# Kernel tuning notes

Measured on AMD Instinct MI355X. Metric: run time of the kernel, lower is better.

Reference implementation:

```python
import jax, jax.numpy as jnp
import numpy as np

B, L, D_MODEL = 4, 4096, 1024
D_STATE = 16
DT_RANK = D_MODEL // 16  # 64
K = 4  # conv kernel size
EPS = 1e-5


def setup_inputs() -> dict:
    key = jax.random.key(0)
    ks = jax.random.split(key, 8)
    s = 0.02
    f = jax.random.normal(ks[0], (B, L, D_MODEL), dtype=jnp.float32)
    ln_g = jnp.ones((D_MODEL,), jnp.float32)
    ln_b = jnp.zeros((D_MODEL,), jnp.float32)
    Wx = jax.random.normal(ks[1], (D_MODEL, D_MODEL), jnp.float32) * s
    bx = jnp.zeros((D_MODEL,), jnp.float32)
    conv_w = jax.random.normal(ks[2], (D_MODEL, K), jnp.float32) * 0.1
    conv_b = jax.random.normal(ks[3], (D_MODEL,), jnp.float32) * s
    Wxp = jax.random.normal(ks[4], (D_MODEL, DT_RANK + 2 * D_STATE), jnp.float32) * s
    Wdt = jax.random.normal(ks[5], (DT_RANK, D_MODEL), jnp.float32) * s
    # negative bias keeps delta small so the (non-exponentiated) recurrence
    # h = (delta*A)*h + ... stays stable over L=4096 steps (|delta*A| < 1)
    bdt = jnp.full((D_MODEL,), -4.0, jnp.float32)
    A_log = jnp.tile(jnp.log(jnp.arange(1, D_STATE + 1, dtype=jnp.float32)), (D_MODEL, 1))
    Dp = jnp.ones((D_MODEL,), jnp.float32)
    return {"f": f, "ln_g": ln_g, "ln_b": ln_b, "Wx": Wx, "bx": bx,
            "conv_w": conv_w, "conv_b": conv_b, "Wxp": Wxp, "Wdt": Wdt,
            "bdt": bdt, "A_log": A_log, "Dp": Dp}


def reference(f, ln_g, ln_b, Wx, bx, conv_w, conv_b, Wxp, Wdt, bdt, A_log, Dp):
    b, l, d = f.shape
    # LayerNorm
    mu = jnp.mean(f, axis=-1, keepdims=True)
    var = jnp.mean(jnp.square(f - mu), axis=-1, keepdims=True)
    fn = (f - mu) * jax.lax.rsqrt(var + EPS) * ln_g + ln_b
    # input projection
    x = fn @ Wx + bx  # (b, l, d)
    # depthwise causal conv1d (torch pad=3 both sides then truncate to l == left-pad 3)
    xp = jnp.pad(x, ((0, 0), (K - 1, 0), (0, 0)))
    windows = jnp.stack([xp[:, k:k + l, :] for k in range(K)], axis=-1)  # (b, l, d, k)
    x = jnp.einsum('bldk,dk->bld', windows, conv_w) + conv_b
    x = jax.nn.silu(x)
    # selective SSM
    x_dbl = x @ Wxp  # (b, l, dt_rank + 2*n)
    dt = x_dbl[..., :DT_RANK]
    Bm = x_dbl[..., DT_RANK:DT_RANK + D_STATE]
    Cm = x_dbl[..., DT_RANK + D_STATE:]
    delta = jax.nn.softplus(dt @ Wdt + bdt)  # (b, l, d)
    A = -jnp.exp(A_log)  # (d, n)

    def step(h, inp):
        d_t, B_t, C_t, x_t = inp  # (b,d) (b,n) (b,n) (b,d)
        dA = d_t[:, :, None] * A                                  # (b, d, n)
        dB = (d_t * x_t)[:, :, None] * B_t[:, None, :]            # (b, d, n)
        h = dA * h + dB
        y = jnp.einsum('bdn,bn->bd', h, C_t)
        return h, y

    h0 = jnp.zeros((b, d, D_STATE), x.dtype)
    xs = (jnp.swapaxes(delta, 0, 1), jnp.swapaxes(Bm, 0, 1),
          jnp.swapaxes(Cm, 0, 1), jnp.swapaxes(x, 0, 1))
    _, ys = jax.lax.scan(step, h0, xs)  # ys: (l, b, d)
    y = jnp.swapaxes(ys, 0, 1) + x * Dp
    return y
```

## Files before the change

kernel.cpp:

```cpp
#include <hip/hip_runtime.h>
#include <cstdint>
#include <cstddef>

#define D_MODEL 1024
#define SEQ_L   4096
#define BATCH   4
#define NROWS   (BATCH*SEQ_L)
#define DSTATE  16
#define DTRANK  64
#define NDBL    96
#define CLEN    64
#define WARM    8
#define CT      16

typedef __attribute__((ext_vector_type(8))) _Float16 f16x8;
typedef __attribute__((ext_vector_type(4))) _Float16 h4;
typedef __attribute__((ext_vector_type(8))) _Float16 h8;
typedef __attribute__((ext_vector_type(4))) float f32x4;
typedef __attribute__((ext_vector_type(2))) float f32x2;

typedef __attribute__((address_space(1))) const unsigned int* as1_u32p;
typedef __attribute__((address_space(3))) unsigned int* as3_u32p;

__device__ __forceinline__ void gload16(const void* g, void* l) {
  __builtin_amdgcn_global_load_lds((as1_u32p)g, (as3_u32p)l, 16, 0, 0);
}

__device__ __forceinline__ float silu(float v) {
  return v / (1.f + __expf(-v));
}

__device__ __forceinline__ float softplus(float z) {
  return (z > 20.f) ? z : __logf(1.f + __expf(z));
}

__device__ __forceinline__ int swz64(int r, int e) { return e ^ ((r & 7) << 3); }

__global__ __launch_bounds__(256) void ln_kernel(const float* __restrict__ f,
                                                 const float* __restrict__ g,
                                                 const float* __restrict__ bta,
                                                 _Float16* __restrict__ fnb) {
  int row = blockIdx.x;
  int tid = threadIdx.x;
  const float* fr = f + (size_t)row * D_MODEL;
  float4 v = *(const float4*)&fr[tid * 4];
  float s  = v.x + v.y + v.z + v.w;
  float ss = v.x*v.x + v.y*v.y + v.z*v.z + v.w*v.w;
  #pragma unroll
  for (int o = 32; o > 0; o >>= 1) { s += __shfl_down(s, o); ss += __shfl_down(ss, o); }
  __shared__ float rs[8];
  int lane = tid & 63, w = tid >> 6;
  if (lane == 0) { rs[w] = s; rs[4 + w] = ss; }
  __syncthreads();
  if (tid == 0) {
    float S = rs[0] + rs[1] + rs[2] + rs[3];
    float SS = rs[4] + rs[5] + rs[6] + rs[7];
    float mu = S * (1.f / D_MODEL);
    float var = SS * (1.f / D_MODEL) - mu * mu;
    rs[0] = mu; rs[1] = rsqrtf(var + 1e-5f);
  }
  __syncthreads();
  float mu = rs[0], rstd = rs[1];
  float4 gv = *(const float4*)&g[tid * 4];
  float4 bv = *(const float4*)&bta[tid * 4];
  h4 o;
  o.x = (_Float16)((v.x - mu) * rstd * gv.x + bv.x);
  o.y = (_Float16)((v.y - mu) * rstd * gv.y + bv.y);
  o.z = (_Float16)((v.z - mu) * rstd * gv.z + bv.z);
  o.w = (_Float16)((v.w - mu) * rstd * gv.w + bv.w);
  *(h4*)&fnb[(size_t)row * D_MODEL + tid * 4] = o;
}

__global__ __launch_bounds__(256) void tcast(const float* __restrict__ W,
                                             _Float16* __restrict__ Wt,
                                             int rows, int cols) {
  __shared__ float tile[32][33];
  int tx = threadIdx.x & 31, ty = threadIdx.x >> 5;
  int c0 = blockIdx.x * 32, r0 = blockIdx.y * 32;
  #pragma unroll
  for (int i = 0; i < 4; ++i) {
    int r = ty + i * 8;
    tile[r][tx] = W[(size_t)(r0 + r) * cols + c0 + tx];
  }
  __syncthreads();
  #pragma unroll
  for (int i = 0; i < 4; ++i) {
    int n = ty + i * 8;
    Wt[(size_t)(c0 + n) * rows + r0 + tx] = (_Float16)tile[tx][n];
  }
}

__global__ __launch_bounds__(256, 4) void gemm1(const _Float16* __restrict__ Ab,
                                                const _Float16* __restrict__ Bt,
                                                const float* __restrict__ bias,
                                                _Float16* __restrict__ C) {
  __shared__ __align__(16) _Float16 As[128 * 64];
  __shared__ __align__(16) _Float16 Bs[128 * 64];
  const int K = D_MODEL, N = D_MODEL;
  int tid = threadIdx.x;
  int row0 = blockIdx.x * 128;
  int col0 = blockIdx.y * 128;
  int wave = tid >> 6, lane = tid & 63;
  int wr = wave >> 1, wc = wave & 1;
  int lr = lane & 15, half = lane >> 4;
  f32x4 acc[4][4] = {};

  int r_[4], sofs[4], ldso[4];
  #pragma unroll
  for (int i = 0; i < 4; ++i) {
    int c = tid + i * 256;
    int r = c >> 3, kc = c & 7;
    r_[i] = r;
    sofs[i] = ((kc ^ (r & 7)) * 8);
    ldso[i] = c * 8;
  }

  for (int ks = 0; ks < 16; ++ks) {
    int k0 = ks * 64;
    __syncthreads();
    #pragma unroll
    for (int i = 0; i < 4; ++i) {
      gload16(&Ab[(size_t)(row0 + r_[i]) * K + k0 + sofs[i]], &As[ldso[i]]);
      gload16(&Bt[(size_t)(col0 + r_[i]) * K + k0 + sofs[i]], &Bs[ldso[i]]);
    }
    __syncthreads();
    #pragma unroll
    for (int kk = 0; kk < 2; ++kk) {
      int kch = ((kk * 4 + half) ^ (lr & 7)) * 8;
      f16x8 a[4], b[4];
      #pragma unroll
      for (int m = 0; m < 4; ++m)
        a[m] = *(const f16x8*)&As[(wr * 64 + m * 16 + lr) * 64 + kch];
      #pragma unroll
      for (int n = 0; n < 4; ++n)
        b[n] = *(const f16x8*)&Bs[(wc * 64 + n * 16 + lr) * 64 + kch];
      #pragma unroll
      for (int m = 0; m < 4; ++m)
        #pragma unroll
        for (int n = 0; n < 4; ++n)
          acc[m][n] = __builtin_amdgcn_mfma_f32_16x16x32_f16(b[n], a[m], acc[m][n], 0, 0, 0);
    }
  }
  #pragma unroll
  for (int m = 0; m < 4; ++m) {
    int gr = row0 + wr * 64 + m * 16 + lr;
    #pragma unroll
    for (int n = 0; n < 4; ++n) {
      int gc = col0 + wc * 64 + n * 16 + half * 4;
      float4 bv4 = *(const float4*)&bias[gc];
      h4 o;
      o.x = (_Float16)(acc[m][n][0] + bv4.x);
      o.y = (_Float16)(acc[m][n][1] + bv4.y);
      o.z = (_Float16)(acc[m][n][2] + bv4.z);
      o.w = (_Float16)(acc[m][n][3] + bv4.w);
      *(h4*)&C[(size_t)gr * N + gc] = o;
    }
  }
}

__global__ __launch_bounds__(256) void conv_silu(const _Float16* __restrict__ xlin,
                                                 const float* __restrict__ cw,
                                                 const float* __restrict__ cb,
                                                 _Float16* __restrict__ xo) {
  int idx = blockIdx.x * 256 + threadIdx.x;
  int d8 = idx & 127;
  int tg = idx >> 7;
  int row0 = tg * CT;
  int l0 = row0 & (SEQ_L - 1);
  int d = d8 * 8;
  float w[8][4];
  #pragma unroll
  for (int j = 0; j < 8; ++j) {
    float4 t = *(const float4*)&cw[(d + j) * 4];
    w[j][0] = t.x; w[j][1] = t.y; w[j][2] = t.z; w[j][3] = t.w;
  }
  float bias[8];
  #pragma unroll
  for (int j = 0; j < 8; j += 4) {
    float4 cbv = *(const float4*)&cb[d + j];
    bias[j] = cbv.x; bias[j+1] = cbv.y; bias[j+2] = cbv.z; bias[j+3] = cbv.w;
  }
  float win0[8], win1[8], win2[8];
  if (l0 == 0) {
    #pragma unroll
    for (int j = 0; j < 8; ++j) { win0[j] = 0.f; win1[j] = 0.f; win2[j] = 0.f; }
  } else {
    h8 m3 = *(const h8*)&xlin[(size_t)(row0 - 3) * D_MODEL + d];
    h8 m2 = *(const h8*)&xlin[(size_t)(row0 - 2) * D_MODEL + d];
    h8 m1 = *(const h8*)&xlin[(size_t)(row0 - 1) * D_MODEL + d];
    #pragma unroll
    for (int j = 0; j < 8; ++j) { win0[j] = (float)m3[j]; win1[j] = (float)m2[j]; win2[j] = (float)m1[j]; }
  }
  #pragma unroll
  for (int tt = 0; tt < CT; tt += 4) {
    h8 ld[4];
    #pragma unroll
    for (int k = 0; k < 4; ++k)
      ld[k] = *(const h8*)&xlin[(size_t)(row0 + tt + k) * D_MODEL + d];
    #pragma unroll
    for (int k = 0; k < 4; ++k) {
      float cur[8];
      #pragma unroll
      for (int j = 0; j < 8; ++j) cur[j] = (float)ld[k][j];
      h8 o;
      #pragma unroll
      for (int j = 0; j < 8; ++j) {
        float v = bias[j] + win0[j]*w[j][0] + win1[j]*w[j][1] + win2[j]*w[j][2] + cur[j]*w[j][3];
        o[j] = (_Float16)silu(v);
      }
      *(h8*)&xo[(size_t)(row0 + tt + k) * D_MODEL + d] = o;
      #pragma unroll
      for (int j = 0; j < 8; ++j) { win0[j] = win1[j]; win1[j] = win2[j]; win2[j] = cur[j]; }
    }
  }
}

__global__ __launch_bounds__(256) void gemm2(const _Float16* __restrict__ X,
                                             const _Float16* __restrict__ WT,
                                             float* __restrict__ Y) {
  __shared__ __align__(16) _Float16 As[64 * 64];
  __shared__ __align__(16) _Float16 Bs[96 * 64];
  int tid = threadIdx.x;
  int row0 = blockIdx.x * 64;
  int wave = tid >> 6, lane = tid & 63;
  int lr = lane & 15, half = lane >> 4;
  f32x4 acc[6] = {};
  for (int k0 = 0; k0 < D_MODEL; k0 += 64) {
    __syncthreads();
    #pragma unroll
    for (int i = 0; i < 2; ++i) {
      int cc = tid + i * 256;
      int r = cc >> 3, ko = (cc & 7) * 8;
      *(h8*)&As[r * 64 + swz64(r, ko)] = *(const h8*)&X[(size_t)(row0 + r) * D_MODEL + k0 + ko];
    }
    #pragma unroll
    for (int i = 0; i < 3; ++i) {
      int cc = tid + i * 256;
      int r = cc >> 3, ko = (cc & 7) * 8;
      *(h8*)&Bs[r * 64 + swz64(r, ko)] = *(const h8*)&WT[(size_t)r * D_MODEL + k0 + ko];
    }
    __syncthreads();
    #pragma unroll
    for (int kk = 0; kk < 2; ++kk) {
      f16x8 a = *(const f16x8*)&As[(wave * 16 + lr) * 64 + swz64(lr, kk * 32 + half * 8)];
      #pragma unroll
      for (int n = 0; n < 6; ++n) {
        f16x8 b = *(const f16x8*)&Bs[(n * 16 + lr) * 64 + swz64(lr, kk * 32 + half * 8)];
        acc[n] = __builtin_amdgcn_mfma_f32_16x16x32_f16(b, a, acc[n], 0, 0, 0);
      }
    }
  }
  int gr = row0 + wave * 16 + lr;
  #pragma unroll
  for (int n = 0; n < 6; ++n) {
    int gc = n * 16 + half * 4;
    *(f32x4*)&Y[(size_t)gr * NDBL + gc] = acc[n];
  }
}

__global__ __launch_bounds__(256) void gemm3(const float* __restrict__ XD,
                                             const _Float16* __restrict__ WT,
                                             const float* __restrict__ bdt,
                                             _Float16* __restrict__ Dl) {
  __shared__ __align__(16) _Float16 As[128 * 64];
  __shared__ __align__(16) _Float16 Bs[128 * 64];
  int tid = threadIdx.x;
  int row0 = blockIdx.x * 128;
  int col0 = blockIdx.y * 128;
  int wave = tid >> 6, lane = tid & 63;
  int wr = wave >> 1, wc = wave & 1;
  int lr = lane & 15, half = lane >> 4;
  #pragma unroll
  for (int i = 0; i < 8; ++i) {
    int cc = tid + i * 256;
    int r = cc >> 4, ko = (cc & 15) * 4;
    float4 v = *(const float4*)&XD[(size_t)(row0 + r) * NDBL + ko];
    h4 o; o.x = (_Float16)v.x; o.y = (_Float16)v.y; o.z = (_Float16)v.z; o.w = (_Float16)v.w;
    *(h4*)&As[r * 64 + swz64(r, ko)] = o;
  }
  #pragma unroll
  for (int i = 0; i < 4; ++i) {
    int cc = tid + i * 256;
    int r = cc >> 3, ko = (cc & 7) * 8;
    *(h8*)&Bs[r * 64 + swz64(r, ko)] = *(const h8*)&WT[(size_t)(col0 + r) * DTRANK + ko];
  }
  __syncthreads();
  f32x4 acc[4][4] = {};
  #pragma unroll
  for (int kk = 0; kk < 2; ++kk) {
    f16x8 a[4], b[4];
    #pragma unroll
    for (int m = 0; m < 4; ++m)
      a[m] = *(const f16x8*)&As[(wr * 64 + m * 16 + lr) * 64 + swz64(lr, kk * 32 + half * 8)];
    #pragma unroll
    for (int n = 0; n < 4; ++n)
      b[n] = *(const f16x8*)&Bs[(wc * 64 + n * 16 + lr) * 64 + swz64(lr, kk * 32 + half * 8)];
    #pragma unroll
    for (int m = 0; m < 4; ++m)
      #pragma unroll
      for (int n = 0; n < 4; ++n)
        acc[m][n] = __builtin_amdgcn_mfma_f32_16x16x32_f16(b[n], a[m], acc[m][n], 0, 0, 0);
  }
  #pragma unroll
  for (int m = 0; m < 4; ++m) {
    int gr = row0 + wr * 64 + m * 16 + lr;
    #pragma unroll
    for (int n = 0; n < 4; ++n) {
      int gc = col0 + wc * 64 + n * 16 + half * 4;
      float4 bv = *(const float4*)&bdt[gc];
      h4 o;
      o.x = (_Float16)softplus(acc[m][n][0] + bv.x);
      o.y = (_Float16)softplus(acc[m][n][1] + bv.y);
      o.z = (_Float16)softplus(acc[m][n][2] + bv.z);
      o.w = (_Float16)softplus(acc[m][n][3] + bv.w);
      *(h4*)&Dl[(size_t)gr * D_MODEL + gc] = o;
    }
  }
}

__global__ __launch_bounds__(256) void scan(const _Float16* __restrict__ delta,
                                            const _Float16* __restrict__ x,
                                            const float* __restrict__ xdbl,
                                            const float* __restrict__ A_log,
                                            const float* __restrict__ Dp,
                                            float* __restrict__ out) {
  int c = blockIdx.x, b = blockIdx.y, dq = blockIdx.z;
  int tid = threadIdx.x;
  int d = dq * 256 + tid;
  int warm = (c == 0) ? 0 : WARM;
  int t0 = c * CLEN - warm;
  int nt = CLEN + warm;
  __shared__ __align__(16) float Bl[(CLEN + WARM) * 16];
  __shared__ __align__(16) float Cl[(CLEN + WARM) * 16];
  int rowbase = b * SEQ_L + t0;
  for (int i = tid; i < nt * 4; i += 256) {
    int t = i >> 2, no = (i & 3) * 4;
    *(float4*)&Bl[t * 16 + no] = *(const float4*)&xdbl[(size_t)(rowbase + t) * NDBL + DTRANK + no];
    *(float4*)&Cl[t * 16 + no] = *(const float4*)&xdbl[(size_t)(rowbase + t) * NDBL + DTRANK + DSTATE + no];
  }
  __syncthreads();
  f32x2 Ar2[8], h2[8];
  #pragma unroll
  for (int q = 0; q < 4; ++q) {
    float4 al = *(const float4*)&A_log[d * 16 + q * 4];
    Ar2[q*2+0] = (f32x2){-__expf(al.x), -__expf(al.y)};
    Ar2[q*2+1] = (f32x2){-__expf(al.z), -__expf(al.w)};
  }
  #pragma unroll
  for (int q = 0; q < 8; ++q) h2[q] = (f32x2){0.f, 0.f};
  float dpv = Dp[d];
  const _Float16* dp_ = delta + (size_t)rowbase * D_MODEL + d;
  const _Float16* xp_ = x + (size_t)rowbase * D_MODEL + d;
  float* op_ = out + (size_t)rowbase * D_MODEL + d;
  const int PF = 8;
  float dnx[PF], xnx[PF];
  #pragma unroll
  for (int k = 0; k < PF; ++k) {
    dnx[k] = (float)dp_[(size_t)k * D_MODEL];
    xnx[k] = (float)xp_[(size_t)k * D_MODEL];
  }
  for (int tb = 0; tb < nt; tb += PF) {
    float dcur[PF], xcur[PF];
    #pragma unroll
    for (int k = 0; k < PF; ++k) { dcur[k] = dnx[k]; xcur[k] = xnx[k]; }
    if (tb + PF < nt) {
      #pragma unroll
      for (int k = 0; k < PF; ++k) {
        dnx[k] = (float)dp_[(size_t)(tb + PF + k) * D_MODEL];
        xnx[k] = (float)xp_[(size_t)(tb + PF + k) * D_MODEL];
      }
    }
    #pragma unroll
    for (int k = 0; k < PF; ++k) {
      int t = tb + k;
      float dlt = dcur[k], xv = xcur[k];
      float dx = dlt * xv;
      f32x2 dlt2 = (f32x2){dlt, dlt};
      f32x2 dx2  = (f32x2){dx, dx};
      f32x2 y2   = (f32x2){0.f, 0.f};
      const float4* Bp = (const float4*)&Bl[t * 16];
      const float4* Cp = (const float4*)&Cl[t * 16];
      #pragma unroll
      for (int q = 0; q < 4; ++q) {
        float4 bq = Bp[q];
        float4 cq = Cp[q];
        f32x2 blo = (f32x2){bq.x, bq.y}, bhi = (f32x2){bq.z, bq.w};
        f32x2 clo = (f32x2){cq.x, cq.y}, chi = (f32x2){cq.z, cq.w};
        f32x2 alo = dlt2 * Ar2[q*2+0];
        f32x2 ahi = dlt2 * Ar2[q*2+1];
        h2[q*2+0] = alo * h2[q*2+0] + dx2 * blo;
        h2[q*2+1] = ahi * h2[q*2+1] + dx2 * bhi;
        y2 = y2 + h2[q*2+0] * clo;
        y2 = y2 + h2[q*2+1] * chi;
      }
      if (t >= warm)
        __builtin_nontemporal_store(y2[0] + y2[1] + xv * dpv, &op_[(size_t)t * D_MODEL]);
    }
  }
}

extern "C" void kernel_launch(void* const* d_in, const int* in_sizes, int n_in,
                              void* d_out, int out_size, void* d_ws, size_t ws_size,
                              hipStream_t stream) {
  const float* f     = (const float*)d_in[0];
  const float* ln_g  = (const float*)d_in[1];
  const float* ln_b  = (const float*)d_in[2];
  const float* Wx    = (const float*)d_in[3];
  const float* bx    = (const float*)d_in[4];
  const float* convw = (const float*)d_in[5];
  const float* convb = (const float*)d_in[6];
  const float* Wxp   = (const float*)d_in[7];
  const float* Wdt   = (const float*)d_in[8];
  const float* bdt   = (const float*)d_in[9];
  const float* A_log = (const float*)d_in[10];
  const float* Dp    = (const float*)d_in[11];
  float* out = (float*)d_out;
  char* ws = (char*)d_ws;

  _Float16* fnb  = (_Float16*)(ws);
  _Float16* xlin = (_Float16*)(ws + 33554432);
  _Float16* xbuf = (_Float16*)(ws + 67108864);
  float*    xdbl = (float*)(ws + 100663296);
  _Float16* wxt  = (_Float16*)(ws + 106954752);
  _Float16* wxpT = (_Float16*)(ws + 109051904);
  _Float16* wdtT = (_Float16*)(ws + 109248512);
  _Float16* delta = xlin;

  tcast<<<dim3(32, 32), dim3(256), 0, stream>>>(Wx, wxt, 1024, 1024);
  tcast<<<dim3(3, 32),  dim3(256), 0, stream>>>(Wxp, wxpT, 1024, 96);
  tcast<<<dim3(32, 2),  dim3(256), 0, stream>>>(Wdt, wdtT, 64, 1024);
  ln_kernel<<<dim3(NROWS), dim3(256), 0, stream>>>(f, ln_g, ln_b, fnb);
  gemm1<<<dim3(NROWS / 128, D_MODEL / 128), dim3(256), 0, stream>>>(fnb, wxt, bx, xlin);
  conv_silu<<<dim3((NROWS / CT) * (D_MODEL / 8) / 256), dim3(256), 0, stream>>>(xlin, convw, convb, xbuf);
  gemm2<<<dim3(NROWS / 64), dim3(256), 0, stream>>>(xbuf, wxpT, xdbl);
  gemm3<<<dim3(NROWS / 128, D_MODEL / 128), dim3(256), 0, stream>>>(xdbl, wdtT, bdt, delta);
  scan<<<dim3(SEQ_L / CLEN, BATCH, 4), dim3(256), 0, stream>>>(delta, xbuf, xdbl, A_log, Dp, out);
}
```

Measured before the change: 158.4 us.

## Split x_dbl into fp16 dt and packed fp32 B/C buffers, merge weight casts

gemm2 now writes the dt part of x_dbl as fp16 into its own buffer and packs B and C into a contiguous 32-float buffer. gemm3 can then stage dt with direct 16-byte global-to-LDS loads using an XOR swizzle, with no fp32-to-fp16 conversion. The scan reads B and C as one packed stream. The three weight transpose-cast launches are merged into a single kernel to cut launch overhead. The dt projection now passes through an fp16 intermediate, which gemm3 already converted to before this change.

```diff
diff --git a/kernel.cpp b/kernel.cpp
--- a/kernel.cpp
+++ b/kernel.cpp
@@ -71,12 +71,20 @@
   *(h4*)&fnb[(size_t)row * D_MODEL + tid * 4] = o;
 }
 
-__global__ __launch_bounds__(256) void tcast(const float* __restrict__ W,
-                                             _Float16* __restrict__ Wt,
-                                             int rows, int cols) {
+__global__ __launch_bounds__(256) void tcast_all(const float* __restrict__ Wx,
+                                                 const float* __restrict__ Wxp,
+                                                 const float* __restrict__ Wdt,
+                                                 _Float16* __restrict__ wxt,
+                                                 _Float16* __restrict__ wxpT,
+                                                 _Float16* __restrict__ wdtT) {
+  int bid = blockIdx.x;
+  const float* W; _Float16* Wt; int rows, cols, bx, by;
+  if (bid < 1024)      { W = Wx;  Wt = wxt;  rows = 1024; cols = 1024; bx = bid & 31;  by = bid >> 5; }
+  else if (bid < 1120) { int b = bid - 1024; W = Wxp; Wt = wxpT; rows = 1024; cols = 96;  bx = b % 3;  by = b / 3; }
+  else                 { int b = bid - 1120; W = Wdt; Wt = wdtT; rows = 64;   cols = 1024; bx = b & 31; by = b >> 5; }
   __shared__ float tile[32][33];
   int tx = threadIdx.x & 31, ty = threadIdx.x >> 5;
-  int c0 = blockIdx.x * 32, r0 = blockIdx.y * 32;
+  int c0 = bx * 32, r0 = by * 32;
   #pragma unroll
   for (int i = 0; i < 4; ++i) {
     int r = ty + i * 8;
@@ -217,7 +225,8 @@
 
 __global__ __launch_bounds__(256) void gemm2(const _Float16* __restrict__ X,
                                              const _Float16* __restrict__ WT,
-                                             float* __restrict__ Y) {
+                                             _Float16* __restrict__ dth,
+                                             float* __restrict__ bc) {
   __shared__ __align__(16) _Float16 As[64 * 64];
   __shared__ __align__(16) _Float16 Bs[96 * 64];
   int tid = threadIdx.x;
@@ -252,13 +261,23 @@
   }
   int gr = row0 + wave * 16 + lr;
   #pragma unroll
-  for (int n = 0; n < 6; ++n) {
+  for (int n = 0; n < 4; ++n) {
     int gc = n * 16 + half * 4;
-    *(f32x4*)&Y[(size_t)gr * NDBL + gc] = acc[n];
-  }
-}
-
-__global__ __launch_bounds__(256) void gemm3(const float* __restrict__ XD,
+    h4 o;
+    o.x = (_Float16)acc[n][0];
+    o.y = (_Float16)acc[n][1];
+    o.z = (_Float16)acc[n][2];
+    o.w = (_Float16)acc[n][3];
+    *(h4*)&dth[(size_t)gr * DTRANK + gc] = o;
+  }
+  #pragma unroll
+  for (int n = 4; n < 6; ++n) {
+    int gc = (n - 4) * 16 + half * 4;
+    *(f32x4*)&bc[(size_t)gr * 32 + gc] = acc[n];
+  }
+}
+
+__global__ __launch_bounds__(256) void gemm3(const _Float16* __restrict__ dth,
                                              const _Float16* __restrict__ WT,
                                              const float* __restrict__ bdt,
                                              _Float16* __restrict__ Dl) {
@@ -271,30 +290,26 @@
   int wr = wave >> 1, wc = wave & 1;
   int lr = lane & 15, half = lane >> 4;
   #pragma unroll
-  for (int i = 0; i < 8; ++i) {
-    int cc = tid + i * 256;
-    int r = cc >> 4, ko = (cc & 15) * 4;
-    float4 v = *(const float4*)&XD[(size_t)(row0 + r) * NDBL + ko];
-    h4 o; o.x = (_Float16)v.x; o.y = (_Float16)v.y; o.z = (_Float16)v.z; o.w = (_Float16)v.w;
-    *(h4*)&As[r * 64 + swz64(r, ko)] = o;
-  }
-  #pragma unroll
   for (int i = 0; i < 4; ++i) {
-    int cc = tid + i * 256;
-    int r = cc >> 3, ko = (cc & 7) * 8;
-    *(h8*)&Bs[r * 64 + swz64(r, ko)] = *(const h8*)&WT[(size_t)(col0 + r) * DTRANK + ko];
+    int c = tid + i * 256;
+    int r = c >> 3, kc = c & 7;
+    int sofs = (kc ^ (r & 7)) * 8;
+    int ldso = c * 8;
+    gload16(&dth[(size_t)(row0 + r) * DTRANK + sofs], &As[ldso]);
+    gload16(&WT[(size_t)(col0 + r) * DTRANK + sofs], &Bs[ldso]);
   }
   __syncthreads();
   f32x4 acc[4][4] = {};
   #pragma unroll
   for (int kk = 0; kk < 2; ++kk) {
+    int kch = ((kk * 4 + half) ^ (lr & 7)) * 8;
     f16x8 a[4], b[4];
     #pragma unroll
     for (int m = 0; m < 4; ++m)
-      a[m] = *(const f16x8*)&As[(wr * 64 + m * 16 + lr) * 64 + swz64(lr, kk * 32 + half * 8)];
+      a[m] = *(const f16x8*)&As[(wr * 64 + m * 16 + lr) * 64 + kch];
     #pragma unroll
     for (int n = 0; n < 4; ++n)
-      b[n] = *(const f16x8*)&Bs[(wc * 64 + n * 16 + lr) * 64 + swz64(lr, kk * 32 + half * 8)];
+      b[n] = *(const f16x8*)&Bs[(wc * 64 + n * 16 + lr) * 64 + kch];
     #pragma unroll
     for (int m = 0; m < 4; ++m)
       #pragma unroll
@@ -320,7 +335,7 @@
 
 __global__ __launch_bounds__(256) void scan(const _Float16* __restrict__ delta,
                                             const _Float16* __restrict__ x,
-                                            const float* __restrict__ xdbl,
+                                            const float* __restrict__ bc,
                                             const float* __restrict__ A_log,
                                             const float* __restrict__ Dp,
                                             float* __restrict__ out) {
@@ -330,13 +345,11 @@
   int warm = (c == 0) ? 0 : WARM;
   int t0 = c * CLEN - warm;
   int nt = CLEN + warm;
-  __shared__ __align__(16) float Bl[(CLEN + WARM) * 16];
-  __shared__ __align__(16) float Cl[(CLEN + WARM) * 16];
+  __shared__ __align__(16) float BCl[(CLEN + WARM) * 32];
   int rowbase = b * SEQ_L + t0;
-  for (int i = tid; i < nt * 4; i += 256) {
-    int t = i >> 2, no = (i & 3) * 4;
-    *(float4*)&Bl[t * 16 + no] = *(const float4*)&xdbl[(size_t)(rowbase + t) * NDBL + DTRANK + no];
-    *(float4*)&Cl[t * 16 + no] = *(const float4*)&xdbl[(size_t)(rowbase + t) * NDBL + DTRANK + DSTATE + no];
+  for (int i = tid; i < nt * 8; i += 256) {
+    int t = i >> 3, no = (i & 7) * 4;
+    *(float4*)&BCl[t * 32 + no] = *(const float4*)&bc[(size_t)(rowbase + t) * 32 + no];
   }
   __syncthreads();
   f32x2 Ar2[8], h2[8];
@@ -378,8 +391,8 @@
       f32x2 dlt2 = (f32x2){dlt, dlt};
       f32x2 dx2  = (f32x2){dx, dx};
       f32x2 y2   = (f32x2){0.f, 0.f};
-      const float4* Bp = (const float4*)&Bl[t * 16];
-      const float4* Cp = (const float4*)&Cl[t * 16];
+      const float4* Bp = (const float4*)&BCl[t * 32];
+      const float4* Cp = (const float4*)&BCl[t * 32 + 16];
       #pragma unroll
       for (int q = 0; q < 4; ++q) {
         float4 bq = Bp[q];
@@ -420,19 +433,18 @@
   _Float16* fnb  = (_Float16*)(ws);
   _Float16* xlin = (_Float16*)(ws + 33554432);
   _Float16* xbuf = (_Float16*)(ws + 67108864);
-  float*    xdbl = (float*)(ws + 100663296);
-  _Float16* wxt  = (_Float16*)(ws + 106954752);
-  _Float16* wxpT = (_Float16*)(ws + 109051904);
-  _Float16* wdtT = (_Float16*)(ws + 109248512);
+  _Float16* dth  = (_Float16*)(ws + 100663296);
+  float*    bc   = (float*)(ws + 102760448);
+  _Float16* wxt  = (_Float16*)(ws + 104857600);
+  _Float16* wxpT = (_Float16*)(ws + 106954752);
+  _Float16* wdtT = (_Float16*)(ws + 107151360);
   _Float16* delta = xlin;
 
-  tcast<<<dim3(32, 32), dim3(256), 0, stream>>>(Wx, wxt, 1024, 1024);
-  tcast<<<dim3(3, 32),  dim3(256), 0, stream>>>(Wxp, wxpT, 1024, 96);
-  tcast<<<dim3(32, 2),  dim3(256), 0, stream>>>(Wdt, wdtT, 64, 1024);
+  tcast_all<<<dim3(1184), dim3(256), 0, stream>>>(Wx, Wxp, Wdt, wxt, wxpT, wdtT);
   ln_kernel<<<dim3(NROWS), dim3(256), 0, stream>>>(f, ln_g, ln_b, fnb);
   gemm1<<<dim3(NROWS / 128, D_MODEL / 128), dim3(256), 0, stream>>>(fnb, wxt, bx, xlin);
   conv_silu<<<dim3((NROWS / CT) * (D_MODEL / 8) / 256), dim3(256), 0, stream>>>(xlin, convw, convb, xbuf);
-  gemm2<<<dim3(NROWS / 64), dim3(256), 0, stream>>>(xbuf, wxpT, xdbl);
-  gemm3<<<dim3(NROWS / 128, D_MODEL / 128), dim3(256), 0, stream>>>(xdbl, wdtT, bdt, delta);
-  scan<<<dim3(SEQ_L / CLEN, BATCH, 4), dim3(256), 0, stream>>>(delta, xbuf, xdbl, A_log, Dp, out);
-}
+  gemm2<<<dim3(NROWS / 64), dim3(256), 0, stream>>>(xbuf, wxpT, dth, bc);
+  gemm3<<<dim3(NROWS / 128, D_MODEL / 128), dim3(256), 0, stream>>>(dth, wdtT, bdt, delta);
+  scan<<<dim3(SEQ_L / CLEN, BATCH, 4), dim3(256), 0, stream>>>(delta, xbuf, bc, A_log, Dp, out);
+}
```

New measurement: 169.3 us, median of 2. +6.9%, slower.
